# Performance work log

Hardware: AMD Instinct MI355X
Metric: run time of the kernel (lower is better)

Reference implementation:

```python
import jax, jax.numpy as jnp
import numpy as np

B, S, D, H = 4, 2048, 1024, 16
DH = D // H  # head dim = 64
MASK_VALUE = -1000000.0


def setup_inputs() -> dict:
    key = jax.random.key(0)
    ks = jax.random.split(key, 8)
    return {
        "key": jax.random.normal(ks[0], (B, S, D), jnp.float32),
        "query": jax.random.normal(ks[1], (B, S, D), jnp.float32),
        "value": jax.random.normal(ks[2], (B, S, D), jnp.float32),
        "valid_lens": jax.random.randint(ks[3], (B,), 0, 2048, jnp.int32),
        # nn.Linear weights stored as [out_features, in_features]
        "Wk": jax.random.normal(ks[4], (D, D), jnp.float32) / np.sqrt(D),
        "Wq": jax.random.normal(ks[5], (D, D), jnp.float32) / np.sqrt(D),
        "Wv": jax.random.normal(ks[6], (D, D), jnp.float32) / np.sqrt(D),
        "Wo": jax.random.normal(ks[7], (D, D), jnp.float32) / np.sqrt(D),
    }


def _split_heads(x):
    # [B, S, D] -> [B, H, S, DH]
    return x.reshape(B, S, H, DH).transpose(0, 2, 1, 3)


def reference(key, query, value, valid_lens, Wk, Wq, Wv, Wo):
    # projections (Linear: x @ W^T, bias=False)
    q = _split_heads(query @ Wq.T)  # [B, H, S, DH]
    k = _split_heads(key @ Wk.T)
    v = _split_heads(value @ Wv.T)

    scale = 1.0 / jnp.sqrt(jnp.asarray(DH, q.dtype))
    scores = jnp.einsum("bhqd,bhkd->bhqk", q, k) * scale  # [B, H, S, S]

    # valid_lens masks the key axis per batch element (same for all heads/queries)
    key_mask = jnp.arange(S) < valid_lens[:, None]  # [B, S]
    scores = jnp.where(key_mask[:, None, None, :], scores, MASK_VALUE)

    attn = jax.nn.softmax(scores, axis=-1)
    out = jnp.einsum("bhqk,bhkd->bhqd", attn, v)  # [B, H, S, DH]
    out = out.transpose(0, 2, 1, 3).reshape(B, S, D)  # concat heads
    return out @ Wo.T
```

## Files before the change

kernel.cpp:

```cpp
#include <hip/hip_runtime.h>
#include <hip/hip_bf16.h>
#include <stdint.h>

typedef __bf16 bf16;
typedef __bf16 bf16x4 __attribute__((ext_vector_type(4)));
typedef __bf16 bf16x8 __attribute__((ext_vector_type(8)));
typedef float f32x4 __attribute__((ext_vector_type(4)));
typedef float f32x8 __attribute__((ext_vector_type(8)));

#define MFMA16 __builtin_amdgcn_mfma_f32_16x16x32_bf16

__device__ __forceinline__ void gload_lds16(void* lds, const void* g) {
  __builtin_amdgcn_global_load_lds(
      (const __attribute__((address_space(1))) unsigned int*)g,
      (__attribute__((address_space(3))) unsigned int*)lds, 16, 0, 0);
}

__global__ __launch_bounds__(256) void cvt3(
    const float* __restrict__ s0, const float* __restrict__ s1,
    const float* __restrict__ s2, bf16* __restrict__ d0,
    bf16* __restrict__ d1, bf16* __restrict__ d2) {
  const float* srcs[3] = {s0, s1, s2};
  bf16* dsts[3] = {d0, d1, d2};
  const float* src = srcs[blockIdx.y];
  bf16* dst = dsts[blockIdx.y];
  int i = (blockIdx.x * 256 + threadIdx.x) * 4;
  f32x4 v = *(const f32x4*)(src + i);
  bf16x4 o;
#pragma unroll
  for (int j = 0; j < 4; j++) o[j] = (bf16)v[j];
  *(bf16x4*)(dst + i) = o;
}

__global__ __launch_bounds__(256) void cvt1(const float* __restrict__ src,
                                            bf16* __restrict__ dst) {
  int i = (blockIdx.x * 256 + threadIdx.x) * 4;
  f32x4 v = *(const f32x4*)(src + i);
  bf16x4 o;
#pragma unroll
  for (int j = 0; j < 4; j++) o[j] = (bf16)v[j];
  *(bf16x4*)(dst + i) = o;
}

__global__ __launch_bounds__(256) void cvt4(const float* __restrict__ w0,
                                            const float* __restrict__ w1,
                                            const float* __restrict__ w2,
                                            const float* __restrict__ w3,
                                            bf16* __restrict__ dst) {
  const float* srcs[4] = {w0, w1, w2, w3};
  const float* src = srcs[blockIdx.y];
  int i = (blockIdx.x * 256 + threadIdx.x) * 4;
  f32x4 v = *(const f32x4*)(src + i);
  bf16x4 o;
#pragma unroll
  for (int j = 0; j < 4; j++) o[j] = (bf16)v[j];
  *(bf16x4*)(dst + (size_t)blockIdx.y * 1048576 + i) = o;
}

__device__ __forceinline__ void xcd_remap(int& m0, int& n0) {
  int id = blockIdx.y * 8 + blockIdx.x;
  int xcd = id & 7;
  int j = id >> 3;
  m0 = (xcd * 8 + (j >> 3)) * 128;
  n0 = (j & 7) * 128;
}

__device__ __forceinline__ void gemm_body(const bf16* __restrict__ A,
                                          const bf16* __restrict__ W,
                                          void* __restrict__ Craw, int mode,
                                          int m0, int n0, bf16* As, bf16* Bs) {
  constexpr int K = 1024;
  const int t = threadIdx.x;
  const int lane = t & 63;
  const int quad = lane >> 4;
  const int m16 = lane & 15;
  const int w = t >> 6;
  const int wm = (w >> 1) * 64;
  const int wn = (w & 1) * 64;

  f32x4 acc[4][4];
#pragma unroll
  for (int i = 0; i < 4; i++)
#pragma unroll
    for (int j = 0; j < 4; j++) acc[i][j] = (f32x4){0.f, 0.f, 0.f, 0.f};

  for (int kt = 0; kt < K / 32; kt++) {
    __syncthreads();
#pragma unroll
    for (int p = 0; p < 2; p++) {
      int idx = p * 256 + t;
      int row = idx >> 2;
      int ce = (idx & 3) * 8;
      gload_lds16(&As[idx * 8], A + (size_t)(m0 + row) * K + kt * 32 + ce);
      gload_lds16(&Bs[idx * 8], W + (size_t)(n0 + row) * K + kt * 32 + ce);
    }
    __syncthreads();

    bf16x8 af[4], bfr[4];
#pragma unroll
    for (int i = 0; i < 4; i++) {
      af[i] = *(const bf16x8*)&As[(wm + i * 16 + m16) * 32 + quad * 8];
      bfr[i] = *(const bf16x8*)&Bs[(wn + i * 16 + m16) * 32 + quad * 8];
    }
#pragma unroll
    for (int i = 0; i < 4; i++)
#pragma unroll
      for (int j = 0; j < 4; j++)
        acc[i][j] = MFMA16(af[i], bfr[j], acc[i][j], 0, 0, 0);
  }

#pragma unroll
  for (int i = 0; i < 4; i++) {
    int rbase = m0 + wm + i * 16 + quad * 4;
#pragma unroll
    for (int j = 0; j < 4; j++) {
      int col = n0 + wn + j * 16 + m16;
#pragma unroll
      for (int r = 0; r < 4; r++) {
        int row = rbase + r;
        if (mode == 0) {
          ((float*)Craw)[(size_t)row * 1024 + col] = acc[i][j][r];
        } else {
          int b = row >> 11, s = row & 2047;
          int h = col >> 6, d = col & 63;
          bf16 v = (bf16)acc[i][j][r];
          if (mode == 1)
            ((bf16*)Craw)[(((size_t)(b * 16 + h)) * 2048 + s) * 64 + d] = v;
          else
            ((bf16*)Craw)[(((size_t)(b * 16 + h)) * 64 + d) * 2048 + s] = v;
        }
      }
    }
  }
}

__global__ __launch_bounds__(256) void gemm_qkv(
    const bf16* __restrict__ xq, const bf16* __restrict__ xk,
    const bf16* __restrict__ xv, const bf16* __restrict__ wb,
    const int* __restrict__ vlen, bf16* __restrict__ qp,
    bf16* __restrict__ kp, bf16* __restrict__ vt) {
  __shared__ bf16 As[128 * 32];
  __shared__ bf16 Bs[128 * 32];
  int m0, n0;
  xcd_remap(m0, n0);
  const int z = blockIdx.z;
  if (z >= 1) {
    int b = m0 >> 11;
    int s0 = m0 & 2047;
    int vl = vlen[b];
    if (vl != 0 && s0 >= vl) return;
  }
  const bf16* A = (z == 0) ? xq : (z == 1) ? xk : xv;
  const bf16* W = wb + (size_t)z * 1048576;
  bf16* C = (z == 0) ? qp : (z == 1) ? kp : vt;
  gemm_body(A, W, C, (z == 2) ? 2 : 1, m0, n0, As, Bs);
}

__global__ __launch_bounds__(256) void gemm_one(const bf16* __restrict__ A,
                                                const bf16* __restrict__ W,
                                                void* __restrict__ Craw,
                                                int mode) {
  __shared__ bf16 As[128 * 32];
  __shared__ bf16 Bs[128 * 32];
  int m0, n0;
  xcd_remap(m0, n0);
  gemm_body(A, W, Craw, mode, m0, n0, As, Bs);
}

template <int AF32, int WF32>
__global__ __launch_bounds__(256) void gemm_bt(const void* __restrict__ Araw,
                                               const void* __restrict__ Wraw,
                                               void* __restrict__ Craw,
                                               int mode) {
  constexpr int K = 1024;
  __shared__ bf16 As[128 * 32];
  __shared__ bf16 Bs[128 * 32];
  const int t = threadIdx.x;
  const int lane = t & 63;
  const int quad = lane >> 4;
  const int m16 = lane & 15;
  const int w = t >> 6;
  const int m0 = blockIdx.y * 128;
  const int n0 = blockIdx.x * 128;
  const int wm = (w >> 1) * 64;
  const int wn = (w & 1) * 64;

  f32x4 acc[4][4];
#pragma unroll
  for (int i = 0; i < 4; i++)
#pragma unroll
    for (int j = 0; j < 4; j++) acc[i][j] = (f32x4){0.f, 0.f, 0.f, 0.f};

  for (int kt = 0; kt < K / 32; kt++) {
    bf16x8 aR[2], bR[2];
#pragma unroll
    for (int p = 0; p < 2; p++) {
      int idx = p * 256 + t;
      int row = idx >> 2;
      int ce = (idx & 3) * 8;
      size_t aoff = (size_t)(m0 + row) * K + kt * 32 + ce;
      size_t boff = (size_t)(n0 + row) * K + kt * 32 + ce;
      if constexpr (AF32) {
        f32x8 av = *(const f32x8*)((const float*)Araw + aoff);
#pragma unroll
        for (int j = 0; j < 8; j++) aR[p][j] = (bf16)av[j];
      } else {
        aR[p] = *(const bf16x8*)((const bf16*)Araw + aoff);
      }
      if constexpr (WF32) {
        f32x8 bv = *(const f32x8*)((const float*)Wraw + boff);
#pragma unroll
        for (int j = 0; j < 8; j++) bR[p][j] = (bf16)bv[j];
      } else {
        bR[p] = *(const bf16x8*)((const bf16*)Wraw + boff);
      }
    }
    __syncthreads();
#pragma unroll
    for (int p = 0; p < 2; p++) {
      int idx = p * 256 + t;
      *(bf16x8*)&As[idx * 8] = aR[p];
      *(bf16x8*)&Bs[idx * 8] = bR[p];
    }
    __syncthreads();

    bf16x8 af[4], bfr[4];
#pragma unroll
    for (int i = 0; i < 4; i++) {
      af[i] = *(const bf16x8*)&As[(wm + i * 16 + m16) * 32 + quad * 8];
      bfr[i] = *(const bf16x8*)&Bs[(wn + i * 16 + m16) * 32 + quad * 8];
    }
#pragma unroll
    for (int i = 0; i < 4; i++)
#pragma unroll
      for (int j = 0; j < 4; j++)
        acc[i][j] = MFMA16(af[i], bfr[j], acc[i][j], 0, 0, 0);
  }

#pragma unroll
  for (int i = 0; i < 4; i++) {
    int rbase = m0 + wm + i * 16 + quad * 4;
#pragma unroll
    for (int j = 0; j < 4; j++) {
      int col = n0 + wn + j * 16 + m16;
#pragma unroll
      for (int r = 0; r < 4; r++) {
        int row = rbase + r;
        if (mode == 0) {
          ((float*)Craw)[(size_t)row * 1024 + col] = acc[i][j][r];
        } else {
          int b = row >> 11, s = row & 2047;
          int h = col >> 6, d = col & 63;
          bf16 v = (bf16)acc[i][j][r];
          if (mode == 1)
            ((bf16*)Craw)[(((size_t)(b * 16 + h)) * 2048 + s) * 64 + d] = v;
          else
            ((bf16*)Craw)[(((size_t)(b * 16 + h)) * 64 + d) * 2048 + s] = v;
        }
      }
    }
  }
}

__global__ __launch_bounds__(256) void attn(const bf16* __restrict__ qp,
                                            const bf16* __restrict__ kp,
                                            const bf16* __restrict__ vt,
                                            const int* __restrict__ vlen,
                                            bf16* __restrict__ ctx) {
  __shared__ bf16 Ks[64 * 64];
  __shared__ bf16 Vs[64 * 64];
  __shared__ bf16 Ps[4 * 32 * 72];

  const int t = threadIdx.x;
  const int lane = t & 63;
  const int quad = lane >> 4;
  const int m16 = lane & 15;
  const int sw = m16 & 7;
  const int w = t >> 6;
  const int bh = blockIdx.y;
  const int qt = blockIdx.x;
  const int b = bh >> 4;
  const int h = bh & 15;
  const int vl = vlen[b];

  const float C1 = 0.18033688f;
  const float C2 = 46.166241f;
  const float mArg = (vl == 0) ? 0.0f : -12800.0f;

  bf16x8 qf[2][2];
#pragma unroll
  for (int a = 0; a < 2; a++) {
    const bf16* qb =
        qp + ((size_t)(bh * 2048 + qt * 128 + w * 32 + a * 16 + m16)) * 64;
    qf[a][0] = *(const bf16x8*)(qb + quad * 8);
    qf[a][1] = *(const bf16x8*)(qb + 32 + quad * 8);
  }

  float rsum[2][4] = {{0.f, 0.f, 0.f, 0.f}, {0.f, 0.f, 0.f, 0.f}};
  f32x4 o[2][4];
#pragma unroll
  for (int a = 0; a < 2; a++)
#pragma unroll
    for (int nt = 0; nt < 4; nt++) o[a][nt] = (f32x4){0.f, 0.f, 0.f, 0.f};

  const int ktEnd = (vl == 0) ? 32 : ((vl + 63) >> 6);

  for (int kt = 0; kt < ktEnd; kt++) {
    __syncthreads();
#pragma unroll
    for (int p = 0; p < 2; p++) {
      int idx = p * 256 + t;
      int row = idx >> 3;
      int gc = (idx & 7) ^ (row & 7);
      gload_lds16(&Ks[idx * 8],
                  &kp[((size_t)(bh * 2048 + kt * 64 + row)) * 64 + gc * 8]);
      gload_lds16(&Vs[idx * 8],
                  &vt[((size_t)(bh * 64 + row)) * 2048 + kt * 64 + gc * 8]);
    }
    __syncthreads();

    f32x4 s[2][4];
#pragma unroll
    for (int a = 0; a < 2; a++)
#pragma unroll
      for (int nt = 0; nt < 4; nt++) s[a][nt] = (f32x4){0.f, 0.f, 0.f, 0.f};
#pragma unroll
    for (int nt = 0; nt < 4; nt++) {
      int key = nt * 16 + m16;
#pragma unroll
      for (int ks = 0; ks < 2; ks++) {
        bf16x8 kf =
            *(const bf16x8*)&Ks[key * 64 + (((ks * 4 + quad) ^ sw) * 8)];
        s[0][nt] = MFMA16(qf[0][ks], kf, s[0][nt], 0, 0, 0);
        s[1][nt] = MFMA16(qf[1][ks], kf, s[1][nt], 0, 0, 0);
      }
    }

#pragma unroll
    for (int nt = 0; nt < 4; nt++) {
      bool masked = (kt * 64 + nt * 16 + m16) >= vl;
#pragma unroll
      for (int a = 0; a < 2; a++)
#pragma unroll
        for (int r = 0; r < 4; r++) {
          float arg = masked ? mArg : (s[a][nt][r] * C1 - C2);
          bf16 pb = (bf16)__builtin_amdgcn_exp2f(arg);
          rsum[a][r] += (float)pb;
          Ps[w * 2304 + (a * 16 + quad * 4 + r) * 72 + nt * 16 + m16] = pb;
        }
    }

#pragma unroll
    for (int ks = 0; ks < 2; ks++) {
      bf16x8 pf0 = *(const bf16x8*)&Ps[w * 2304 + m16 * 72 + ks * 32 + quad * 8];
      bf16x8 pf1 =
          *(const bf16x8*)&Ps[w * 2304 + (16 + m16) * 72 + ks * 32 + quad * 8];
#pragma unroll
      for (int nt = 0; nt < 4; nt++) {
        int dh = nt * 16 + m16;
        bf16x8 vf =
            *(const bf16x8*)&Vs[dh * 64 + (((ks * 4 + quad) ^ sw) * 8)];
        o[0][nt] = MFMA16(pf0, vf, o[0][nt], 0, 0, 0);
        o[1][nt] = MFMA16(pf1, vf, o[1][nt], 0, 0, 0);
      }
    }
  }

#pragma unroll
  for (int off = 1; off < 16; off <<= 1)
#pragma unroll
    for (int a = 0; a < 2; a++)
#pragma unroll
      for (int r = 0; r < 4; r++) rsum[a][r] += __shfl_xor(rsum[a][r], off);
#pragma unroll
  for (int a = 0; a < 2; a++)
#pragma unroll
    for (int r = 0; r < 4; r++) rsum[a][r] = 1.0f / rsum[a][r];

#pragma unroll
  for (int a = 0; a < 2; a++)
#pragma unroll
    for (int nt = 0; nt < 4; nt++) {
      int dh = nt * 16 + m16;
#pragma unroll
      for (int r = 0; r < 4; r++) {
        int srow = qt * 128 + w * 32 + a * 16 + quad * 4 + r;
        ctx[((size_t)(b * 2048 + srow)) * 1024 + h * 64 + dh] =
            (bf16)(o[a][nt][r] * rsum[a][r]);
      }
    }
}

extern "C" void kernel_launch(void* const* d_in, const int* in_sizes, int n_in,
                              void* d_out, int out_size, void* d_ws,
                              size_t ws_size, hipStream_t stream) {
  const float* key = (const float*)d_in[0];
  const float* query = (const float*)d_in[1];
  const float* value = (const float*)d_in[2];
  const int* vlen = (const int*)d_in[3];
  const float* Wk = (const float*)d_in[4];
  const float* Wq = (const float*)d_in[5];
  const float* Wv = (const float*)d_in[6];
  const float* Wo = (const float*)d_in[7];

  const size_t NE = (size_t)4 * 2048 * 1024;
  const size_t WE = 1048576;

  const size_t needA = (6 * NE + 4 * WE) * sizeof(bf16);
  const size_t needB = (5 * NE + 4 * WE) * sizeof(bf16);
  dim3 gg(8, 64), gb(256);

  if (ws_size >= needA) {
    bf16* qp = (bf16*)d_ws;
    bf16* kp = qp + NE;
    bf16* vt = kp + NE;
    bf16* xq = vt + NE;
    bf16* xk = xq + NE;
    bf16* xv = xk + NE;
    bf16* wb = xv + NE;
    bf16* ctx = xq;

    cvt4<<<dim3(1024, 4), gb, 0, stream>>>(Wq, Wk, Wv, Wo, wb);
    cvt3<<<dim3(8192, 3), gb, 0, stream>>>(query, key, value, xq, xk, xv);
    gemm_qkv<<<dim3(8, 64, 3), gb, 0, stream>>>(xq, xk, xv, wb, vlen, qp, kp,
                                                vt);
    attn<<<dim3(16, 64), gb, 0, stream>>>(qp, kp, vt, vlen, ctx);
    gemm_one<<<gg, gb, 0, stream>>>(ctx, wb + 3 * WE, d_out, 0);
  } else if (ws_size >= needB) {
    bf16* qp = (bf16*)d_ws;
    bf16* kp = qp + NE;
    bf16* vt = kp + NE;
    bf16* ctx = vt + NE;
    bf16* xb = ctx + NE;
    bf16* wb = xb + NE;

    cvt4<<<dim3(1024, 4), gb, 0, stream>>>(Wq, Wk, Wv, Wo, wb);
    cvt1<<<8192, gb, 0, stream>>>(query, xb);
    gemm_one<<<gg, gb, 0, stream>>>(xb, wb + 0 * WE, qp, 1);
    cvt1<<<8192, gb, 0, stream>>>(key, xb);
    gemm_one<<<gg, gb, 0, stream>>>(xb, wb + 1 * WE, kp, 1);
    cvt1<<<8192, gb, 0, stream>>>(value, xb);
    gemm_one<<<gg, gb, 0, stream>>>(xb, wb + 2 * WE, vt, 2);
    attn<<<dim3(16, 64), gb, 0, stream>>>(qp, kp, vt, vlen, ctx);
    gemm_one<<<gg, gb, 0, stream>>>(ctx, wb + 3 * WE, d_out, 0);
  } else {
    bf16* qp = (bf16*)d_ws;
    bf16* kp = qp + NE;
    bf16* vt = kp + NE;
    bf16* ctx = vt + NE;
    gemm_bt<1, 1><<<gg, gb, 0, stream>>>(query, Wq, qp, 1);
    gemm_bt<1, 1><<<gg, gb, 0, stream>>>(key, Wk, kp, 1);
    gemm_bt<1, 1><<<gg, gb, 0, stream>>>(value, Wv, vt, 2);
    attn<<<dim3(16, 64), gb, 0, stream>>>(qp, kp, vt, vlen, ctx);
    gemm_bt<0, 1><<<gg, gb, 0, stream>>>(ctx, Wo, d_out, 0);
  }
}
```

Measured before the change: 334.0 us.

## Replace 128x128 GEMMs with 256x256 double-buffered, swizzled, 8-warp pipelined GEMM

The projection GEMMs move from 128x128 tiles with a K step of 32 and two full syncthreads per step to 256x256 tiles with a K step of 64. They now run 512 threads per block, double-buffer LDS in 128 KB, and XOR-swizzle the LDS layout. Global-to-LDS loads are interleaved with the MFMA phases using explicit vmcnt/lgkmcnt waits, s_barrier and setprio, so loads overlap compute and each tile is reused more. In exchange the block grid shrinks, which may under-fill the CUs, and the hand-written barrier schedule is fragile if it is wrong.

```diff
diff --git a/kernel.cpp b/kernel.cpp
--- a/kernel.cpp
+++ b/kernel.cpp
@@ -15,6 +15,14 @@
       (const __attribute__((address_space(1))) unsigned int*)g,
       (__attribute__((address_space(3))) unsigned int*)lds, 16, 0, 0);
 }
+
+#define S_BARRIER() __builtin_amdgcn_s_barrier()
+#define WAIT_LGKM0()                                   \
+  do {                                                 \
+    asm volatile("s_waitcnt lgkmcnt(0)" ::: "memory"); \
+    __builtin_amdgcn_sched_barrier(0);                 \
+  } while (0)
+#define WAIT_VM(n) asm volatile("s_waitcnt vmcnt(" #n ")" ::: "memory")
 
 __global__ __launch_bounds__(256) void cvt3(
     const float* __restrict__ s0, const float* __restrict__ s1,
@@ -57,73 +65,193 @@
   *(bf16x4*)(dst + (size_t)blockIdx.y * 1048576 + i) = o;
 }
 
-__device__ __forceinline__ void xcd_remap(int& m0, int& n0) {
-  int id = blockIdx.y * 8 + blockIdx.x;
-  int xcd = id & 7;
-  int j = id >> 3;
-  m0 = (xcd * 8 + (j >> 3)) * 128;
-  n0 = (j & 7) * 128;
-}
-
-__device__ __forceinline__ void gemm_body(const bf16* __restrict__ A,
-                                          const bf16* __restrict__ W,
-                                          void* __restrict__ Craw, int mode,
-                                          int m0, int n0, bf16* As, bf16* Bs) {
+__device__ __forceinline__ void gemm256_body(const bf16* __restrict__ A,
+                                             const bf16* __restrict__ W,
+                                             void* __restrict__ Craw, int mode,
+                                             int m0, int n0, bf16* smem) {
   constexpr int K = 1024;
   const int t = threadIdx.x;
   const int lane = t & 63;
-  const int quad = lane >> 4;
   const int m16 = lane & 15;
+  const int quad = (lane >> 4) & 3;
+  const int sw = m16 & 7;
   const int w = t >> 6;
-  const int wm = (w >> 1) * 64;
-  const int wn = (w & 1) * 64;
-
-  f32x4 acc[4][4];
-#pragma unroll
-  for (int i = 0; i < 4; i++)
-#pragma unroll
-    for (int j = 0; j < 4; j++) acc[i][j] = (f32x4){0.f, 0.f, 0.f, 0.f};
-
-  for (int kt = 0; kt < K / 32; kt++) {
-    __syncthreads();
-#pragma unroll
-    for (int p = 0; p < 2; p++) {
-      int idx = p * 256 + t;
-      int row = idx >> 2;
-      int ce = (idx & 3) * 8;
-      gload_lds16(&As[idx * 8], A + (size_t)(m0 + row) * K + kt * 32 + ce);
-      gload_lds16(&Bs[idx * 8], W + (size_t)(n0 + row) * K + kt * 32 + ce);
-    }
-    __syncthreads();
-
-    bf16x8 af[4], bfr[4];
-#pragma unroll
-    for (int i = 0; i < 4; i++) {
-      af[i] = *(const bf16x8*)&As[(wm + i * 16 + m16) * 32 + quad * 8];
-      bfr[i] = *(const bf16x8*)&Bs[(wn + i * 16 + m16) * 32 + quad * 8];
-    }
-#pragma unroll
-    for (int i = 0; i < 4; i++)
-#pragma unroll
-      for (int j = 0; j < 4; j++)
-        acc[i][j] = MFMA16(af[i], bfr[j], acc[i][j], 0, 0, 0);
-  }
-
-#pragma unroll
-  for (int i = 0; i < 4; i++) {
-    int rbase = m0 + wm + i * 16 + quad * 4;
-#pragma unroll
-    for (int j = 0; j < 4; j++) {
-      int col = n0 + wn + j * 16 + m16;
+  const int wm2 = (w >> 2) * 64;
+  const int wn4 = (w & 3) * 32;
+
+  const bf16* Ab = A + (size_t)m0 * K;
+  const bf16* Bb = W + (size_t)n0 * K;
+
+  auto STG = [&](int buf, int isB, int half, int kt) {
+    bf16* dst = smem + buf * 32768 + isB * 16384 + half * 8192;
+    const bf16* src = (isB ? Bb : Ab) + (size_t)(half * 128) * K + kt * 64;
+#pragma unroll
+    for (int ld = 0; ld < 2; ld++) {
+      int idx = ld * 512 + t;
+      int row = idx >> 3;
+      int c = (idx & 7) ^ (row & 7);
+      gload_lds16(dst + idx * 8, src + (size_t)row * K + c * 8);
+    }
+  };
+
+  bf16x8 aR[8], bR0[4], bR1[4];
+
+  auto LDA = [&](int buf, int half) {
+    const bf16* As = smem + buf * 32768 + half * 8192;
+#pragma unroll
+    for (int f = 0; f < 4; f++)
+#pragma unroll
+      for (int ks = 0; ks < 2; ks++)
+        aR[f * 2 + ks] = *(const bf16x8*)&As[(wm2 + f * 16 + m16) * 64 +
+                                             (((ks * 4 + quad) ^ sw) * 8)];
+  };
+  auto LDB = [&](int buf, int half, bf16x8* bR) {
+    const bf16* Bs = smem + buf * 32768 + 16384 + half * 8192;
+#pragma unroll
+    for (int g = 0; g < 2; g++)
+#pragma unroll
+      for (int ks = 0; ks < 2; ks++)
+        bR[g * 2 + ks] = *(const bf16x8*)&Bs[(wn4 + g * 16 + m16) * 64 +
+                                             (((ks * 4 + quad) ^ sw) * 8)];
+  };
+
+  f32x4 acc[8][4];
+#pragma unroll
+  for (int f = 0; f < 8; f++)
+#pragma unroll
+    for (int g = 0; g < 4; g++) acc[f][g] = (f32x4){0.f, 0.f, 0.f, 0.f};
+
+  auto MM = [&](int mh, int nh, const bf16x8* bR) {
+    __builtin_amdgcn_s_setprio(1);
+#pragma unroll
+    for (int f = 0; f < 4; f++)
+#pragma unroll
+      for (int g = 0; g < 2; g++)
+#pragma unroll
+        for (int ks = 0; ks < 2; ks++)
+          acc[mh * 4 + f][nh * 2 + g] = MFMA16(
+              aR[f * 2 + ks], bR[g * 2 + ks], acc[mh * 4 + f][nh * 2 + g],
+              0, 0, 0);
+    __builtin_amdgcn_s_setprio(0);
+  };
+
+  STG(0, 0, 0, 0);
+  STG(0, 1, 0, 0);
+  STG(0, 0, 1, 0);
+  STG(0, 1, 1, 0);
+  STG(1, 0, 0, 1);
+  STG(1, 1, 0, 1);
+  STG(1, 0, 1, 1);
+  WAIT_VM(6);
+  S_BARRIER();
+
+#pragma unroll 1
+  for (int it = 0; it < 7; ++it) {
+    int t2 = 2 * it + 2, t3 = 2 * it + 3;
+    LDA(0, 0);
+    LDB(0, 0, bR0);
+    STG(1, 1, 1, 2 * it + 1);
+    S_BARRIER();
+    WAIT_LGKM0();
+    MM(0, 0, bR0);
+    S_BARRIER();
+    LDB(0, 1, bR1);
+    STG(0, 0, 0, t2);
+    S_BARRIER();
+    WAIT_LGKM0();
+    MM(0, 1, bR1);
+    S_BARRIER();
+    LDA(0, 1);
+    STG(0, 1, 0, t2);
+    S_BARRIER();
+    WAIT_LGKM0();
+    MM(1, 1, bR1);
+    S_BARRIER();
+    STG(0, 0, 1, t2);
+    S_BARRIER();
+    MM(1, 0, bR0);
+    WAIT_VM(6);
+    S_BARRIER();
+    LDA(1, 0);
+    LDB(1, 0, bR0);
+    STG(0, 1, 1, t2);
+    S_BARRIER();
+    WAIT_LGKM0();
+    MM(0, 0, bR0);
+    S_BARRIER();
+    LDB(1, 1, bR1);
+    STG(1, 0, 0, t3);
+    S_BARRIER();
+    WAIT_LGKM0();
+    MM(0, 1, bR1);
+    S_BARRIER();
+    LDA(1, 1);
+    STG(1, 1, 0, t3);
+    S_BARRIER();
+    WAIT_LGKM0();
+    MM(1, 1, bR1);
+    S_BARRIER();
+    STG(1, 0, 1, t3);
+    S_BARRIER();
+    MM(1, 0, bR0);
+    WAIT_VM(6);
+    S_BARRIER();
+  }
+
+  LDA(0, 0);
+  LDB(0, 0, bR0);
+  STG(1, 1, 1, 15);
+  S_BARRIER();
+  WAIT_LGKM0();
+  MM(0, 0, bR0);
+  S_BARRIER();
+  LDB(0, 1, bR1);
+  S_BARRIER();
+  WAIT_LGKM0();
+  MM(0, 1, bR1);
+  S_BARRIER();
+  LDA(0, 1);
+  S_BARRIER();
+  WAIT_LGKM0();
+  MM(1, 1, bR1);
+  S_BARRIER();
+  S_BARRIER();
+  MM(1, 0, bR0);
+  WAIT_VM(0);
+  S_BARRIER();
+  LDA(1, 0);
+  LDB(1, 0, bR0);
+  S_BARRIER();
+  WAIT_LGKM0();
+  MM(0, 0, bR0);
+  S_BARRIER();
+  LDB(1, 1, bR1);
+  S_BARRIER();
+  WAIT_LGKM0();
+  MM(0, 1, bR1);
+  S_BARRIER();
+  LDA(1, 1);
+  S_BARRIER();
+  WAIT_LGKM0();
+  MM(1, 1, bR1);
+  S_BARRIER();
+  MM(1, 0, bR0);
+
+#pragma unroll
+  for (int f = 0; f < 8; f++) {
+    int rbase = m0 + (f >> 2) * 128 + wm2 + (f & 3) * 16 + quad * 4;
+#pragma unroll
+    for (int g = 0; g < 4; g++) {
+      int col = n0 + (g >> 1) * 128 + wn4 + (g & 1) * 16 + m16;
 #pragma unroll
       for (int r = 0; r < 4; r++) {
         int row = rbase + r;
         if (mode == 0) {
-          ((float*)Craw)[(size_t)row * 1024 + col] = acc[i][j][r];
+          ((float*)Craw)[(size_t)row * 1024 + col] = acc[f][g][r];
         } else {
           int b = row >> 11, s = row & 2047;
           int h = col >> 6, d = col & 63;
-          bf16 v = (bf16)acc[i][j][r];
+          bf16 v = (bf16)acc[f][g][r];
           if (mode == 1)
             ((bf16*)Craw)[(((size_t)(b * 16 + h)) * 2048 + s) * 64 + d] = v;
           else
@@ -134,15 +262,22 @@
   }
 }
 
-__global__ __launch_bounds__(256) void gemm_qkv(
+__device__ __forceinline__ void xcd_remap256(int& m0, int& n0) {
+  int id = blockIdx.y * 4 + blockIdx.x;
+  int xcd = id & 7;
+  int j = id >> 3;
+  m0 = (xcd * 4 + (j >> 2)) * 256;
+  n0 = (j & 3) * 256;
+}
+
+__global__ __launch_bounds__(512, 2) void gemm_qkv(
     const bf16* __restrict__ xq, const bf16* __restrict__ xk,
     const bf16* __restrict__ xv, const bf16* __restrict__ wb,
     const int* __restrict__ vlen, bf16* __restrict__ qp,
     bf16* __restrict__ kp, bf16* __restrict__ vt) {
-  __shared__ bf16 As[128 * 32];
-  __shared__ bf16 Bs[128 * 32];
+  __shared__ bf16 smem[65536];
   int m0, n0;
-  xcd_remap(m0, n0);
+  xcd_remap256(m0, n0);
   const int z = blockIdx.z;
   if (z >= 1) {
     int b = m0 >> 11;
@@ -153,18 +288,16 @@
   const bf16* A = (z == 0) ? xq : (z == 1) ? xk : xv;
   const bf16* W = wb + (size_t)z * 1048576;
   bf16* C = (z == 0) ? qp : (z == 1) ? kp : vt;
-  gemm_body(A, W, C, (z == 2) ? 2 : 1, m0, n0, As, Bs);
-}
-
-__global__ __launch_bounds__(256) void gemm_one(const bf16* __restrict__ A,
-                                                const bf16* __restrict__ W,
-                                                void* __restrict__ Craw,
-                                                int mode) {
-  __shared__ bf16 As[128 * 32];
-  __shared__ bf16 Bs[128 * 32];
+  gemm256_body(A, W, C, (z == 2) ? 2 : 1, m0, n0, smem);
+}
+
+__global__ __launch_bounds__(512, 2) void gemm_one256(
+    const bf16* __restrict__ A, const bf16* __restrict__ W,
+    void* __restrict__ Craw, int mode) {
+  __shared__ bf16 smem[65536];
   int m0, n0;
-  xcd_remap(m0, n0);
-  gemm_body(A, W, Craw, mode, m0, n0, As, Bs);
+  xcd_remap256(m0, n0);
+  gemm256_body(A, W, Craw, mode, m0, n0, smem);
 }
 
 template <int AF32, int WF32>
@@ -408,7 +541,7 @@
 
   const size_t needA = (6 * NE + 4 * WE) * sizeof(bf16);
   const size_t needB = (5 * NE + 4 * WE) * sizeof(bf16);
-  dim3 gg(8, 64), gb(256);
+  dim3 gg(4, 32), gb(512), cb(256);
 
   if (ws_size >= needA) {
     bf16* qp = (bf16*)d_ws;
@@ -420,12 +553,12 @@
     bf16* wb = xv + NE;
     bf16* ctx = xq;
 
-    cvt4<<<dim3(1024, 4), gb, 0, stream>>>(Wq, Wk, Wv, Wo, wb);
-    cvt3<<<dim3(8192, 3), gb, 0, stream>>>(query, key, value, xq, xk, xv);
-    gemm_qkv<<<dim3(8, 64, 3), gb, 0, stream>>>(xq, xk, xv, wb, vlen, qp, kp,
+    cvt4<<<dim3(1024, 4), cb, 0, stream>>>(Wq, Wk, Wv, Wo, wb);
+    cvt3<<<dim3(8192, 3), cb, 0, stream>>>(query, key, value, xq, xk, xv);
+    gemm_qkv<<<dim3(4, 32, 3), gb, 0, stream>>>(xq, xk, xv, wb, vlen, qp, kp,
                                                 vt);
-    attn<<<dim3(16, 64), gb, 0, stream>>>(qp, kp, vt, vlen, ctx);
-    gemm_one<<<gg, gb, 0, stream>>>(ctx, wb + 3 * WE, d_out, 0);
+    attn<<<dim3(16, 64), cb, 0, stream>>>(qp, kp, vt, vlen, ctx);
+    gemm_one256<<<gg, gb, 0, stream>>>(ctx, wb + 3 * WE, d_out, 0);
   } else if (ws_size >= needB) {
     bf16* qp = (bf16*)d_ws;
     bf16* kp = qp + NE;
@@ -434,24 +567,25 @@
     bf16* xb = ctx + NE;
     bf16* wb = xb + NE;
 
-    cvt4<<<dim3(1024, 4), gb, 0, stream>>>(Wq, Wk, Wv, Wo, wb);
-    cvt1<<<8192, gb, 0, stream>>>(query, xb);
-    gemm_one<<<gg, gb, 0, stream>>>(xb, wb + 0 * WE, qp, 1);
-    cvt1<<<8192, gb, 0, stream>>>(key, xb);
-    gemm_one<<<gg, gb, 0, stream>>>(xb, wb + 1 * WE, kp, 1);
-    cvt1<<<8192, gb, 0, stream>>>(value, xb);
-    gemm_one<<<gg, gb, 0, stream>>>(xb, wb + 2 * WE, vt, 2);
-    attn<<<dim3(16, 64), gb, 0, stream>>>(qp, kp, vt, vlen, ctx);
-    gemm_one<<<gg, gb, 0, stream>>>(ctx, wb + 3 * WE, d_out, 0);
+    cvt4<<<dim3(1024, 4), cb, 0, stream>>>(Wq, Wk, Wv, Wo, wb);
+    cvt1<<<8192, cb, 0, stream>>>(query, xb);
+    gemm_one256<<<gg, gb, 0, stream>>>(xb, wb + 0 * WE, qp, 1);
+    cvt1<<<8192, cb, 0, stream>>>(key, xb);
+    gemm_one256<<<gg, gb, 0, stream>>>(xb, wb + 1 * WE, kp, 1);
+    cvt1<<<8192, cb, 0, stream>>>(value, xb);
+    gemm_one256<<<gg, gb, 0, stream>>>(xb, wb + 2 * WE, vt, 2);
+    attn<<<dim3(16, 64), cb, 0, stream>>>(qp, kp, vt, vlen, ctx);
+    gemm_one256<<<gg, gb, 0, stream>>>(ctx, wb + 3 * WE, d_out, 0);
   } else {
     bf16* qp = (bf16*)d_ws;
     bf16* kp = qp + NE;
     bf16* vt = kp + NE;
     bf16* ctx = vt + NE;
-    gemm_bt<1, 1><<<gg, gb, 0, stream>>>(query, Wq, qp, 1);
-    gemm_bt<1, 1><<<gg, gb, 0, stream>>>(key, Wk, kp, 1);
-    gemm_bt<1, 1><<<gg, gb, 0, stream>>>(value, Wv, vt, 2);
-    attn<<<dim3(16, 64), gb, 0, stream>>>(qp, kp, vt, vlen, ctx);
-    gemm_bt<0, 1><<<gg, gb, 0, stream>>>(ctx, Wo, d_out, 0);
-  }
-}
+    dim3 g8(8, 64), b256(256);
+    gemm_bt<1, 1><<<g8, b256, 0, stream>>>(query, Wq, qp, 1);
+    gemm_bt<1, 1><<<g8, b256, 0, stream>>>(key, Wk, kp, 1);
+    gemm_bt<1, 1><<<g8, b256, 0, stream>>>(value, Wv, vt, 2);
+    attn<<<dim3(16, 64), b256, 0, stream>>>(qp, kp, vt, vlen, ctx);
+    gemm_bt<0, 1><<<g8, b256, 0, stream>>>(ctx, Wo, d_out, 0);
+  }
+}
```

After: 344.5 us. 3.1% more time.

## Rewrite projection GEMMs with triple-buffered swizzled LDS pipeline and larger tiles

Applied to the files above, without the earlier changes.

Replaces the single-buffered 128x128xK32 GEMM body with a 128x256xK64 tile run by 512 threads. It triple-buffers LDS through async global-to-LDS loads, uses explicit vmcnt and lgkmcnt waits with barriers, and XOR-swizzles columns to avoid bank conflicts. The goal is to overlap global loads with MFMA work and cut the sync overhead per K step. The cost is much larger LDS use (144KB per block), which limits occupancy. The XCD remap is dropped, so L2 locality across chiplets may change.

```diff
diff --git a/kernel.cpp b/kernel.cpp
--- a/kernel.cpp
+++ b/kernel.cpp
@@ -15,6 +15,14 @@
       (const __attribute__((address_space(1))) unsigned int*)g,
       (__attribute__((address_space(3))) unsigned int*)lds, 16, 0, 0);
 }
+
+#define S_BARRIER() __builtin_amdgcn_s_barrier()
+#define WAIT_LGKM0()                                   \
+  do {                                                 \
+    asm volatile("s_waitcnt lgkmcnt(0)" ::: "memory"); \
+    __builtin_amdgcn_sched_barrier(0);                 \
+  } while (0)
+#define WAIT_VM(n) asm volatile("s_waitcnt vmcnt(" #n ")" ::: "memory")
 
 __global__ __launch_bounds__(256) void cvt3(
     const float* __restrict__ s0, const float* __restrict__ s1,
@@ -57,73 +65,123 @@
   *(bf16x4*)(dst + (size_t)blockIdx.y * 1048576 + i) = o;
 }
 
-__device__ __forceinline__ void xcd_remap(int& m0, int& n0) {
-  int id = blockIdx.y * 8 + blockIdx.x;
-  int xcd = id & 7;
-  int j = id >> 3;
-  m0 = (xcd * 8 + (j >> 3)) * 128;
-  n0 = (j & 7) * 128;
-}
-
-__device__ __forceinline__ void gemm_body(const bf16* __restrict__ A,
-                                          const bf16* __restrict__ W,
-                                          void* __restrict__ Craw, int mode,
-                                          int m0, int n0, bf16* As, bf16* Bs) {
+__device__ __forceinline__ void gemmF_body(const bf16* __restrict__ A,
+                                           const bf16* __restrict__ W,
+                                           void* __restrict__ Craw, int mode,
+                                           int m0, int n0, bf16* smem) {
   constexpr int K = 1024;
   const int t = threadIdx.x;
   const int lane = t & 63;
-  const int quad = lane >> 4;
   const int m16 = lane & 15;
+  const int quad = (lane >> 4) & 3;
+  const int sw = m16 & 7;
   const int w = t >> 6;
-  const int wm = (w >> 1) * 64;
-  const int wn = (w & 1) * 64;
+  const int wm = (w >> 2) * 64;
+  const int wn = (w & 3) * 64;
+
+  const bf16* Ab = A + (size_t)m0 * K;
+  const bf16* Bb = W + (size_t)n0 * K;
+
+  auto STG = [&](int buf, int kt) {
+    bf16* dA = smem + buf * 24576;
+    bf16* dB = dA + 8192;
+    const bf16* sA = Ab + kt * 64;
+    const bf16* sB = Bb + kt * 64;
+#pragma unroll
+    for (int ld = 0; ld < 2; ld++) {
+      int idx = ld * 512 + t;
+      int row = idx >> 3;
+      int c = (idx & 7) ^ (row & 7);
+      gload_lds16(dA + idx * 8, sA + (size_t)row * K + c * 8);
+    }
+#pragma unroll
+    for (int ld = 0; ld < 4; ld++) {
+      int idx = ld * 512 + t;
+      int row = idx >> 3;
+      int c = (idx & 7) ^ (row & 7);
+      gload_lds16(dB + idx * 8, sB + (size_t)row * K + c * 8);
+    }
+  };
+
+  bf16x8 aR[8], bR[8];
+  auto LD = [&](int buf) {
+    const bf16* As = smem + buf * 24576;
+    const bf16* Bs = As + 8192;
+#pragma unroll
+    for (int f = 0; f < 4; f++)
+#pragma unroll
+      for (int ks = 0; ks < 2; ks++) {
+        aR[f * 2 + ks] = *(const bf16x8*)&As[(wm + f * 16 + m16) * 64 +
+                                             (((ks * 4 + quad) ^ sw) * 8)];
+        bR[f * 2 + ks] = *(const bf16x8*)&Bs[(wn + f * 16 + m16) * 64 +
+                                             (((ks * 4 + quad) ^ sw) * 8)];
+      }
+  };
 
   f32x4 acc[4][4];
 #pragma unroll
-  for (int i = 0; i < 4; i++)
-#pragma unroll
-    for (int j = 0; j < 4; j++) acc[i][j] = (f32x4){0.f, 0.f, 0.f, 0.f};
-
-  for (int kt = 0; kt < K / 32; kt++) {
-    __syncthreads();
-#pragma unroll
-    for (int p = 0; p < 2; p++) {
-      int idx = p * 256 + t;
-      int row = idx >> 2;
-      int ce = (idx & 3) * 8;
-      gload_lds16(&As[idx * 8], A + (size_t)(m0 + row) * K + kt * 32 + ce);
-      gload_lds16(&Bs[idx * 8], W + (size_t)(n0 + row) * K + kt * 32 + ce);
-    }
-    __syncthreads();
-
-    bf16x8 af[4], bfr[4];
-#pragma unroll
-    for (int i = 0; i < 4; i++) {
-      af[i] = *(const bf16x8*)&As[(wm + i * 16 + m16) * 32 + quad * 8];
-      bfr[i] = *(const bf16x8*)&Bs[(wn + i * 16 + m16) * 32 + quad * 8];
-    }
-#pragma unroll
-    for (int i = 0; i < 4; i++)
-#pragma unroll
-      for (int j = 0; j < 4; j++)
-        acc[i][j] = MFMA16(af[i], bfr[j], acc[i][j], 0, 0, 0);
-  }
-
-#pragma unroll
-  for (int i = 0; i < 4; i++) {
-    int rbase = m0 + wm + i * 16 + quad * 4;
-#pragma unroll
-    for (int j = 0; j < 4; j++) {
-      int col = n0 + wn + j * 16 + m16;
+  for (int f = 0; f < 4; f++)
+#pragma unroll
+    for (int g = 0; g < 4; g++) acc[f][g] = (f32x4){0.f, 0.f, 0.f, 0.f};
+
+  auto MM = [&]() {
+    __builtin_amdgcn_s_setprio(1);
+#pragma unroll
+    for (int f = 0; f < 4; f++)
+#pragma unroll
+      for (int g = 0; g < 4; g++)
+#pragma unroll
+        for (int ks = 0; ks < 2; ks++)
+          acc[f][g] = MFMA16(aR[f * 2 + ks], bR[g * 2 + ks], acc[f][g], 0, 0, 0);
+    __builtin_amdgcn_s_setprio(0);
+  };
+
+  STG(0, 0);
+  STG(1, 1);
+  WAIT_VM(6);
+  S_BARRIER();
+
+  int bufR = 0;
+#pragma unroll 1
+  for (int kt = 0; kt < 14; ++kt) {
+    LD(bufR);
+    int bufS = bufR + 2;
+    if (bufS >= 3) bufS -= 3;
+    STG(bufS, kt + 2);
+    S_BARRIER();
+    WAIT_LGKM0();
+    MM();
+    WAIT_VM(6);
+    S_BARRIER();
+    bufR = (bufR + 1 == 3) ? 0 : bufR + 1;
+  }
+  LD(bufR);
+  S_BARRIER();
+  WAIT_LGKM0();
+  MM();
+  WAIT_VM(0);
+  S_BARRIER();
+  bufR = (bufR + 1 == 3) ? 0 : bufR + 1;
+  LD(bufR);
+  S_BARRIER();
+  WAIT_LGKM0();
+  MM();
+
+#pragma unroll
+  for (int f = 0; f < 4; f++) {
+    int rbase = m0 + wm + f * 16 + quad * 4;
+#pragma unroll
+    for (int g = 0; g < 4; g++) {
+      int col = n0 + wn + g * 16 + m16;
 #pragma unroll
       for (int r = 0; r < 4; r++) {
         int row = rbase + r;
         if (mode == 0) {
-          ((float*)Craw)[(size_t)row * 1024 + col] = acc[i][j][r];
+          ((float*)Craw)[(size_t)row * 1024 + col] = acc[f][g][r];
         } else {
           int b = row >> 11, s = row & 2047;
           int h = col >> 6, d = col & 63;
-          bf16 v = (bf16)acc[i][j][r];
+          bf16 v = (bf16)acc[f][g][r];
           if (mode == 1)
             ((bf16*)Craw)[(((size_t)(b * 16 + h)) * 2048 + s) * 64 + d] = v;
           else
@@ -134,15 +192,14 @@
   }
 }
 
-__global__ __launch_bounds__(256) void gemm_qkv(
+__global__ __launch_bounds__(512, 2) void gemm_qkv(
     const bf16* __restrict__ xq, const bf16* __restrict__ xk,
     const bf16* __restrict__ xv, const bf16* __restrict__ wb,
     const int* __restrict__ vlen, bf16* __restrict__ qp,
     bf16* __restrict__ kp, bf16* __restrict__ vt) {
-  __shared__ bf16 As[128 * 32];
-  __shared__ bf16 Bs[128 * 32];
-  int m0, n0;
-  xcd_remap(m0, n0);
+  __shared__ bf16 smem[73728];
+  const int m0 = blockIdx.y * 128;
+  const int n0 = blockIdx.x * 256;
   const int z = blockIdx.z;
   if (z >= 1) {
     int b = m0 >> 11;
@@ -153,18 +210,15 @@
   const bf16* A = (z == 0) ? xq : (z == 1) ? xk : xv;
   const bf16* W = wb + (size_t)z * 1048576;
   bf16* C = (z == 0) ? qp : (z == 1) ? kp : vt;
-  gemm_body(A, W, C, (z == 2) ? 2 : 1, m0, n0, As, Bs);
-}
-
-__global__ __launch_bounds__(256) void gemm_one(const bf16* __restrict__ A,
-                                                const bf16* __restrict__ W,
-                                                void* __restrict__ Craw,
-                                                int mode) {
-  __shared__ bf16 As[128 * 32];
-  __shared__ bf16 Bs[128 * 32];
-  int m0, n0;
-  xcd_remap(m0, n0);
-  gemm_body(A, W, Craw, mode, m0, n0, As, Bs);
+  gemmF_body(A, W, C, (z == 2) ? 2 : 1, m0, n0, smem);
+}
+
+__global__ __launch_bounds__(512, 2) void gemm_one(const bf16* __restrict__ A,
+                                                   const bf16* __restrict__ W,
+                                                   void* __restrict__ Craw,
+                                                   int mode) {
+  __shared__ bf16 smem[73728];
+  gemmF_body(A, W, Craw, mode, blockIdx.y * 128, blockIdx.x * 256, smem);
 }
 
 template <int AF32, int WF32>
@@ -408,7 +462,7 @@
 
   const size_t needA = (6 * NE + 4 * WE) * sizeof(bf16);
   const size_t needB = (5 * NE + 4 * WE) * sizeof(bf16);
-  dim3 gg(8, 64), gb(256);
+  dim3 gg(4, 64), gb(512), cb(256);
 
   if (ws_size >= needA) {
     bf16* qp = (bf16*)d_ws;
@@ -420,11 +474,11 @@
     bf16* wb = xv + NE;
     bf16* ctx = xq;
 
-    cvt4<<<dim3(1024, 4), gb, 0, stream>>>(Wq, Wk, Wv, Wo, wb);
-    cvt3<<<dim3(8192, 3), gb, 0, stream>>>(query, key, value, xq, xk, xv);
-    gemm_qkv<<<dim3(8, 64, 3), gb, 0, stream>>>(xq, xk, xv, wb, vlen, qp, kp,
+    cvt4<<<dim3(1024, 4), cb, 0, stream>>>(Wq, Wk, Wv, Wo, wb);
+    cvt3<<<dim3(8192, 3), cb, 0, stream>>>(query, key, value, xq, xk, xv);
+    gemm_qkv<<<dim3(4, 64, 3), gb, 0, stream>>>(xq, xk, xv, wb, vlen, qp, kp,
                                                 vt);
-    attn<<<dim3(16, 64), gb, 0, stream>>>(qp, kp, vt, vlen, ctx);
+    attn<<<dim3(16, 64), cb, 0, stream>>>(qp, kp, vt, vlen, ctx);
     gemm_one<<<gg, gb, 0, stream>>>(ctx, wb + 3 * WE, d_out, 0);
   } else if (ws_size >= needB) {
     bf16* qp = (bf16*)d_ws;
@@ -434,24 +488,25 @@
     bf16* xb = ctx + NE;
     bf16* wb = xb + NE;
 
-    cvt4<<<dim3(1024, 4), gb, 0, stream>>>(Wq, Wk, Wv, Wo, wb);
-    cvt1<<<8192, gb, 0, stream>>>(query, xb);
+    cvt4<<<dim3(1024, 4), cb, 0, stream>>>(Wq, Wk, Wv, Wo, wb);
+    cvt1<<<8192, cb, 0, stream>>>(query, xb);
     gemm_one<<<gg, gb, 0, stream>>>(xb, wb + 0 * WE, qp, 1);
-    cvt1<<<8192, gb, 0, stream>>>(key, xb);
+    cvt1<<<8192, cb, 0, stream>>>(key, xb);
     gemm_one<<<gg, gb, 0, stream>>>(xb, wb + 1 * WE, kp, 1);
-    cvt1<<<8192, gb, 0, stream>>>(value, xb);
+    cvt1<<<8192, cb, 0, stream>>>(value, xb);
     gemm_one<<<gg, gb, 0, stream>>>(xb, wb + 2 * WE, vt, 2);
-    attn<<<dim3(16, 64), gb, 0, stream>>>(qp, kp, vt, vlen, ctx);
+    attn<<<dim3(16, 64), cb, 0, stream>>>(qp, kp, vt, vlen, ctx);
     gemm_one<<<gg, gb, 0, stream>>>(ctx, wb + 3 * WE, d_out, 0);
   } else {
     bf16* qp = (bf16*)d_ws;
     bf16* kp = qp + NE;
     bf16* vt = kp + NE;
     bf16* ctx = vt + NE;
-    gemm_bt<1, 1><<<gg, gb, 0, stream>>>(query, Wq, qp, 1);
-    gemm_bt<1, 1><<<gg, gb, 0, stream>>>(key, Wk, kp, 1);
-    gemm_bt<1, 1><<<gg, gb, 0, stream>>>(value, Wv, vt, 2);
-    attn<<<dim3(16, 64), gb, 0, stream>>>(qp, kp, vt, vlen, ctx);
-    gemm_bt<0, 1><<<gg, gb, 0, stream>>>(ctx, Wo, d_out, 0);
-  }
-}
+    dim3 g8(8, 64), b256(256);
+    gemm_bt<1, 1><<<g8, b256, 0, stream>>>(query, Wq, qp, 1);
+    gemm_bt<1, 1><<<g8, b256, 0, stream>>>(key, Wk, kp, 1);
+    gemm_bt<1, 1><<<g8, b256, 0, stream>>>(value, Wv, vt, 2);
+    attn<<<dim3(16, 64), b256, 0, stream>>>(qp, kp, vt, vlen, ctx);
+    gemm_bt<0, 1><<<g8, b256, 0, stream>>>(ctx, Wo, d_out, 0);
+  }
+}
```

Result: faster. 320.7 us (-4.0%).
